# Kernel tuning notes

Hardware: AMD Instinct MI355X
Metric: run time of the kernel (lower is better)

The kernel has to match this reference:

```python
import jax, jax.numpy as jnp
import numpy as np

EPS = 1e-8


def setup_inputs() -> dict:
    key = jax.random.key(0)
    k1, k2, k3 = jax.random.split(key, 3)
    B, K, L, D = 4, 64, 128, 768
    context = jax.random.normal(k1, (B, K, 2, L, D), dtype=jnp.float32)
    # MlpModule(input_size=D): Linear(D, D) -> ReLU -> Linear(D, 1)
    w1 = jax.random.normal(k2, (D, D), dtype=jnp.float32) * (1.0 / np.sqrt(D))
    b1 = jnp.zeros((D,), dtype=jnp.float32)
    w2 = jax.random.normal(k3, (D, 1), dtype=jnp.float32) * (1.0 / np.sqrt(D))
    b2 = jnp.zeros((1,), dtype=jnp.float32)
    return {"context": context, "w1": w1, "b1": b1, "w2": w2, "b2": b2}


def reference(context, w1, b1, w2, b2):
    # context: [B, K, 2, L, D]; slice 0 = context tokens, slice 1 = entity tokens
    ctx = context[:, :, 0, :, :]   # [B, K, L, D]
    ent = context[:, :, 1, :, :]   # [B, K, L, D]

    ctx_norm = jnp.linalg.norm(ctx, axis=-1, keepdims=True)  # [B, K, L, 1]
    ent_norm = jnp.linalg.norm(ent, axis=-1, keepdims=True)  # [B, K, L, 1]

    # cosine-similarity score matrix: [B, K, L, L]
    denom = ctx_norm * jnp.swapaxes(ent_norm, -1, -2) + EPS
    scores = jnp.einsum('bkld,bkmd->bklm', ctx, ent) / denom

    # normalized embeddings (torch code does in-place /= before the stack)
    ctx_n = ctx / ctx_norm
    ent_n = ent / ent_norm

    # top-1 match along entity axis, gather matched entity token per context token
    argmax_idx = jnp.argmax(scores, axis=-1)                       # [B, K, L] int
    matched = jnp.take_along_axis(ent_n, argmax_idx[..., None], axis=2)  # [B, K, L, D]

    pair = jnp.stack([ctx_n, matched], axis=-2)  # [B, K, L, 2, D]

    # MLP: Linear(D,D) -> ReLU -> Linear(D,1), then sum over the pair axis
    h = jax.nn.relu(jnp.einsum('bklpd,de->bklpe', pair, w1) + b1)
    out = jnp.einsum('bklpd,do->bklpo', h, w2) + b2   # [B, K, L, 2, 1]
    out = jnp.sum(out, axis=-2)                        # [B, K, L, 1]
    return jnp.squeeze(out, axis=-1)                   # [B, K, L]
```

## Files before the change

### kernel.cpp

```cpp
#include <hip/hip_runtime.h>
#include <hip/hip_bf16.h>
#include <stdint.h>

#define NB 4
#define NK 64
#define NL 128
#define ND 768
#define NBK (NB*NK)
#define NROW (NBK*NL)
#define LD2 (NL*ND)
#define EPSF 1e-8f
#define THETA 2e-3f
#define CAP 16384

typedef __bf16 bf16x8 __attribute__((ext_vector_type(8)));
typedef float  f32x4  __attribute__((ext_vector_type(4)));

__device__ __forceinline__ int row_off(int r) {
  if (r < NROW) return r*ND + (r >> 7)*LD2;
  int r2 = r - NROW;
  return r2*ND + (r2 >> 7)*LD2 + LD2;
}

__global__ __launch_bounds__(256) void k0_w1t(const float* __restrict__ w1,
                                              __bf16* __restrict__ w1t,
                                              unsigned long long* __restrict__ amax2,
                                              unsigned* __restrict__ cntg) {
  __shared__ float tile[64][68];
  int idx = blockIdx.x*256 + threadIdx.x;
  if (idx < NROW) amax2[idx] = 0ull;
  if (idx == 0) *cntg = 0u;
  int kb = (blockIdx.x / 12) * 64, eb = (blockIdx.x % 12) * 64;
  int t = threadIdx.x;
  int r = t >> 2, c0 = (t & 3) * 16;
  #pragma unroll
  for (int j = 0; j < 4; j++) {
    f32x4 v = *(const f32x4*)(w1 + (kb + r)*ND + eb + c0 + j*4);
    *(f32x4*)&tile[r][c0 + j*4] = v;
  }
  __syncthreads();
  int e = t & 63, gi = t >> 6;
  int eg = eb + e;
  #pragma unroll
  for (int g2 = 0; g2 < 2; g2++) {
    int g = gi*2 + g2;
    bf16x8 o;
    #pragma unroll
    for (int j = 0; j < 8; j++) o[j] = (__bf16)tile[g*8 + j][e];
    int G = (kb >> 3) + (g ^ (eg & 7));
    *(bf16x8*)(w1t + eg*ND + G*8) = o;
  }
}

__device__ __forceinline__ void cvt4(f32x4 v, unsigned& hp0, unsigned& hp1,
                                     unsigned& lp0, unsigned& lp1, float& sq) {
  unsigned u0 = __float_as_uint(v[0]), u1 = __float_as_uint(v[1]);
  unsigned u2 = __float_as_uint(v[2]), u3 = __float_as_uint(v[3]);
  hp0 = (u1 & 0xffff0000u) | (u0 >> 16);
  hp1 = (u3 & 0xffff0000u) | (u2 >> 16);
  float l0 = v[0] - __uint_as_float(u0 & 0xffff0000u);
  float l1 = v[1] - __uint_as_float(u1 & 0xffff0000u);
  float l2 = v[2] - __uint_as_float(u2 & 0xffff0000u);
  float l3 = v[3] - __uint_as_float(u3 & 0xffff0000u);
  lp0 = (__float_as_uint(l1) & 0xffff0000u) | (__float_as_uint(l0) >> 16);
  lp1 = (__float_as_uint(l3) & 0xffff0000u) | (__float_as_uint(l2) >> 16);
  sq += v[0]*v[0] + v[1]*v[1] + v[2]*v[2] + v[3]*v[3];
}

__global__ __launch_bounds__(512) void k2a_screen(
    const float* __restrict__ ctxall, float* __restrict__ norm,
    int* __restrict__ amax, unsigned* __restrict__ cntg,
    unsigned* __restrict__ list) {
  __shared__ alignas(16) __bf16 tiles[2][4][128*32];
  __shared__ float einv_s[128];
  int bk = blockIdx.x;
  int t = threadIdx.x;
  int mat = t >> 8, row = (t >> 1) & 127, kh = (t & 1) * 16;
  const float* src = ctxall + bk*2*LD2 + mat*LD2 + row*ND + kh;
  int w = t >> 6, lane = t & 63, quad = lane >> 4, eloc = lane & 15;

  f32x4 pv[4];
  #pragma unroll
  for (int i = 0; i < 4; i++) pv[i] = *(const f32x4*)(src + i*4);
  float sq = 0.f;
  f32x4 acc[8];
  #pragma unroll
  for (int ct = 0; ct < 8; ct++) acc[ct] = (f32x4){0,0,0,0};

  int p = 0;
  for (int kt = 0; kt < 24; kt++) {
    unsigned h0,h1,h2,h3, l0,l1,l2,l3;
    cvt4(pv[0], h0, h1, l0, l1, sq);
    cvt4(pv[1], h2, h3, l2, l3, sq);
    __bf16* hdst = &tiles[p][2*mat  ][row*32 + kh];
    __bf16* ldst = &tiles[p][2*mat+1][row*32 + kh];
    *(uint4*)hdst = make_uint4(h0,h1,h2,h3);
    *(uint4*)ldst = make_uint4(l0,l1,l2,l3);
    cvt4(pv[2], h0, h1, l0, l1, sq);
    cvt4(pv[3], h2, h3, l2, l3, sq);
    *((uint4*)hdst + 1) = make_uint4(h0,h1,h2,h3);
    *((uint4*)ldst + 1) = make_uint4(l0,l1,l2,l3);
    __syncthreads();
    if (kt < 23) {
      const float* s2 = src + (kt+1)*32;
      #pragma unroll
      for (int i = 0; i < 4; i++) pv[i] = *(const f32x4*)(s2 + i*4);
    }
    bf16x8 ah = *(const bf16x8*)&tiles[p][0][(w*16+eloc)*32 + quad*8];
    bf16x8 al = *(const bf16x8*)&tiles[p][1][(w*16+eloc)*32 + quad*8];
    #pragma unroll
    for (int ct = 0; ct < 8; ct++) {
      bf16x8 bh = *(const bf16x8*)&tiles[p][2][(ct*16+eloc)*32 + quad*8];
      bf16x8 bl = *(const bf16x8*)&tiles[p][3][(ct*16+eloc)*32 + quad*8];
      acc[ct] = __builtin_amdgcn_mfma_f32_16x16x32_bf16(al, bh, acc[ct], 0, 0, 0);
      acc[ct] = __builtin_amdgcn_mfma_f32_16x16x32_bf16(ah, bl, acc[ct], 0, 0, 0);
      acc[ct] = __builtin_amdgcn_mfma_f32_16x16x32_bf16(ah, bh, acc[ct], 0, 0, 0);
    }
    p ^= 1;
  }

  float stot = sq + __shfl_xor(sq, 1);
  if ((t & 1) == 0) {
    float n = sqrtf(stot);
    if (mat == 0) norm[bk*NL + row] = n;
    else { norm[NROW + bk*NL + row] = n; einv_s[row] = 1.0f / n; }
  }
  __syncthreads();

  #pragma unroll
  for (int rr = 0; rr < 4; rr++) {
    float sc[8];
    float best = -3.0e38f; int bcol = 0;
    #pragma unroll
    for (int ct = 0; ct < 8; ct++) {
      sc[ct] = acc[ct][rr] * einv_s[ct*16 + eloc];
      int col = ct*16 + eloc;
      if (sc[ct] > best) { best = sc[ct]; bcol = col; }
    }
    #pragma unroll
    for (int m = 1; m < 16; m <<= 1) {
      float ov = __shfl_xor(best, m);
      int   oc = __shfl_xor(bcol, m);
      if (ov > best || (ov == best && oc < bcol)) { best = ov; bcol = oc; }
    }
    int grow = bk*NL + w*16 + quad*4 + rr;
    if (eloc == 0) amax[grow] = bcol;
    int cnt = 0;
    #pragma unroll
    for (int ct = 0; ct < 8; ct++) cnt += (sc[ct] >= best - THETA) ? 1 : 0;
    #pragma unroll
    for (int m = 1; m < 16; m <<= 1) cnt += __shfl_xor(cnt, m);
    if (cnt >= 2) {
      #pragma unroll
      for (int ct = 0; ct < 8; ct++) {
        if (sc[ct] >= best - THETA) {
          unsigned idx = atomicAdd(cntg, 1u);
          if (idx < CAP) list[idx] = ((unsigned)grow << 7) | (unsigned)(ct*16 + eloc);
        }
      }
    }
  }
}

__global__ __launch_bounds__(256) void k2b_rescore(
    const float* __restrict__ ctxall, const float* __restrict__ norm,
    const unsigned* __restrict__ cntg, const unsigned* __restrict__ list,
    unsigned long long* __restrict__ amax2) {
  unsigned n = *cntg; if (n > CAP) n = CAP;
  int lane = threadIdx.x & 63;
  unsigned wv = blockIdx.x*4 + (threadIdx.x >> 6);
  for (unsigned e = wv; e < n; e += 256) {
    unsigned ent = list[e];
    int row = (int)(ent >> 7), col = (int)(ent & 127);
    int bk = row >> 7;
    const float* a = ctxall + row_off(row);
    const float* b = ctxall + bk*2*LD2 + LD2 + col*ND;
    float d = 0.f;
    #pragma unroll
    for (int i = 0; i < 3; i++) {
      f32x4 va = *(const f32x4*)(a + lane*12 + i*4);
      f32x4 vb = *(const f32x4*)(b + lane*12 + i*4);
      d += va[0]*vb[0] + va[1]*vb[1] + va[2]*vb[2] + va[3]*vb[3];
    }
    #pragma unroll
    for (int m = 1; m < 64; m <<= 1) d += __shfl_xor(d, m);
    if (lane == 0) {
      float cn = norm[row], en = norm[NROW + bk*NL + col];
      float s = d / (cn*en + EPSF);
      unsigned su = __float_as_uint(s);
      unsigned ord = (su & 0x80000000u) ? ~su : (su | 0x80000000u);
      unsigned long long key = ((unsigned long long)ord << 32) | (unsigned)(127 - col);
      atomicMax(&amax2[row], key);
    }
  }
}

__global__ __launch_bounds__(256, 2) void k3_mlp(
    const float* __restrict__ ctxall, const float* __restrict__ norm,
    const __bf16* __restrict__ w1t, const float* __restrict__ b1,
    const float* __restrict__ w2, float* __restrict__ val) {
  __shared__ alignas(16) __bf16 btile[2][16*768];
  int tid = threadIdx.x;
  int wave = tid >> 6, lane = tid & 63;
  int quad = lane >> 4, eloc = lane & 15;
  int rbase = blockIdx.x*128 + wave*32;

  #pragma unroll
  for (int i = 0; i < 6; i++) {
    __builtin_amdgcn_global_load_lds(
      (const __attribute__((address_space(1))) unsigned int*)(w1t + (i*256 + tid)*8),
      (__attribute__((address_space(3))) unsigned int*)(&btile[0][0] + (i*256 + tid)*8),
      16, 0, 0);
  }

  bf16x8 afrag[2][24];
  #pragma unroll
  for (int s = 0; s < 2; s++) {
    int r = rbase + s*16 + eloc;
    const float* src = ctxall + row_off(r);
    float rinv = 1.0f / norm[r];
    #pragma unroll
    for (int ks = 0; ks < 24; ks++) {
      const float* sp = src + ks*32 + quad*8;
      f32x4 v0 = *(const f32x4*)sp;
      f32x4 v1 = *(const f32x4*)(sp + 4);
      bf16x8 a;
      a[0] = (__bf16)(v0[0]*rinv); a[1] = (__bf16)(v0[1]*rinv);
      a[2] = (__bf16)(v0[2]*rinv); a[3] = (__bf16)(v0[3]*rinv);
      a[4] = (__bf16)(v1[0]*rinv); a[5] = (__bf16)(v1[1]*rinv);
      a[6] = (__bf16)(v1[2]*rinv); a[7] = (__bf16)(v1[3]*rinv);
      afrag[s][ks] = a;
    }
  }

  float oacc[2][4] = {{0,0,0,0},{0,0,0,0}};
  int p = 0;
  for (int nt = 0; nt < 48; nt++) {
    __syncthreads();
    if (nt < 47) {
      const __bf16* gsrc = w1t + (nt+1)*16*ND;
      #pragma unroll
      for (int i = 0; i < 6; i++) {
        __builtin_amdgcn_global_load_lds(
          (const __attribute__((address_space(1))) unsigned int*)(gsrc + (i*256 + tid)*8),
          (__attribute__((address_space(3))) unsigned int*)(&btile[p^1][0] + (i*256 + tid)*8),
          16, 0, 0);
      }
    }
    f32x4 h0 = {0,0,0,0}, h1 = {0,0,0,0};
    #pragma unroll
    for (int ks = 0; ks < 24; ks++) {
      int g = ks*4 + quad;
      bf16x8 bfrag = *(const bf16x8*)(&btile[p][0] + eloc*ND + ((g ^ (eloc & 7))*8));
      h0 = __builtin_amdgcn_mfma_f32_16x16x32_bf16(afrag[0][ks], bfrag, h0, 0, 0, 0);
      h1 = __builtin_amdgcn_mfma_f32_16x16x32_bf16(afrag[1][ks], bfrag, h1, 0, 0, 0);
    }
    float b1v = b1[nt*16 + eloc];
    float w2v = w2[nt*16 + eloc];
    #pragma unroll
    for (int rr = 0; rr < 4; rr++) {
      oacc[0][rr] += fmaxf(h0[rr] + b1v, 0.f) * w2v;
      oacc[1][rr] += fmaxf(h1[rr] + b1v, 0.f) * w2v;
    }
    p ^= 1;
  }
  #pragma unroll
  for (int m = 1; m < 16; m <<= 1)
    #pragma unroll
    for (int s = 0; s < 2; s++)
      #pragma unroll
      for (int rr = 0; rr < 4; rr++)
        oacc[s][rr] += __shfl_xor(oacc[s][rr], m);
  if (eloc == 0) {
    #pragma unroll
    for (int s = 0; s < 2; s++)
      #pragma unroll
      for (int rr = 0; rr < 4; rr++)
        val[rbase + s*16 + quad*4 + rr] = oacc[s][rr];
  }
}

__global__ void k4_out(const float* __restrict__ val, const int* __restrict__ amax,
                       const unsigned long long* __restrict__ amax2,
                       const float* __restrict__ b2, float* __restrict__ out) {
  int i = blockIdx.x*256 + threadIdx.x;
  int bk = i >> 7;
  unsigned long long k = amax2[i];
  int a = k ? (127 - (int)(k & 127ull)) : amax[i];
  out[i] = val[i] + val[NROW + bk*NL + a] + 2.0f*b2[0];
}

extern "C" void kernel_launch(void* const* d_in, const int* in_sizes, int n_in,
                              void* d_out, int out_size, void* d_ws, size_t ws_size,
                              hipStream_t stream) {
  const float* ctxall = (const float*)d_in[0];
  const float* w1 = (const float*)d_in[1];
  const float* b1 = (const float*)d_in[2];
  const float* w2 = (const float*)d_in[3];
  const float* b2 = (const float*)d_in[4];
  float* out = (float*)d_out;

  char* ws = (char*)d_ws;
  float*    norm = (float*)ws;
  int*      amax = (int*)(ws + 262144);
  float*    val  = (float*)(ws + 393216);
  __bf16*   w1t  = (__bf16*)(ws + 655360);
  unsigned long long* amax2 = (unsigned long long*)(ws + 1835008);
  unsigned* cntg = (unsigned*)(ws + 2097152);
  unsigned* list = (unsigned*)(ws + 2097156);

  hipLaunchKernelGGL(k0_w1t,     dim3(144),        dim3(256), 0, stream, w1, w1t, amax2, cntg);
  hipLaunchKernelGGL(k2a_screen, dim3(NBK),        dim3(512), 0, stream, ctxall, norm, amax, cntg, list);
  hipLaunchKernelGGL(k2b_rescore,dim3(64),         dim3(256), 0, stream, ctxall, norm, cntg, list, amax2);
  hipLaunchKernelGGL(k3_mlp,     dim3(2*NROW/128), dim3(256), 0, stream, ctxall, norm, w1t, b1, w2, val);
  hipLaunchKernelGGL(k4_out,     dim3(NROW/256),   dim3(256), 0, stream, val, amax, amax2, b2, out);
}
```

Before: 397.7 us.

## Emit bf16 copy of activations in screen kernel and feed MLP from it

New measurement: 431.7 us. 1.09x slower.

```diff
diff --git a/kernel.cpp b/kernel.cpp
--- a/kernel.cpp
+++ b/kernel.cpp
@@ -67,10 +67,17 @@
   sq += v[0]*v[0] + v[1]*v[1] + v[2]*v[2] + v[3]*v[3];
 }
 
+__device__ __forceinline__ bf16x8 rnd8(f32x4 a, f32x4 b) {
+  bf16x8 o;
+  o[0] = (__bf16)a[0]; o[1] = (__bf16)a[1]; o[2] = (__bf16)a[2]; o[3] = (__bf16)a[3];
+  o[4] = (__bf16)b[0]; o[5] = (__bf16)b[1]; o[6] = (__bf16)b[2]; o[7] = (__bf16)b[3];
+  return o;
+}
+
 __global__ __launch_bounds__(512) void k2a_screen(
     const float* __restrict__ ctxall, float* __restrict__ norm,
     int* __restrict__ amax, unsigned* __restrict__ cntg,
-    unsigned* __restrict__ list) {
+    unsigned* __restrict__ list, __bf16* __restrict__ abf16) {
   __shared__ alignas(16) __bf16 tiles[2][4][128*32];
   __shared__ float einv_s[128];
   int bk = blockIdx.x;
@@ -78,6 +85,8 @@
   int mat = t >> 8, row = (t >> 1) & 127, kh = (t & 1) * 16;
   const float* src = ctxall + bk*2*LD2 + mat*LD2 + row*ND + kh;
   int w = t >> 6, lane = t & 63, quad = lane >> 4, eloc = lane & 15;
+  __bf16* arow = abf16 ? (abf16 + (size_t)((mat ? NROW : 0) + bk*NL + row)*ND + kh)
+                       : (__bf16*)0;
 
   f32x4 pv[4];
   #pragma unroll
@@ -96,11 +105,18 @@
     __bf16* ldst = &tiles[p][2*mat+1][row*32 + kh];
     *(uint4*)hdst = make_uint4(h0,h1,h2,h3);
     *(uint4*)ldst = make_uint4(l0,l1,l2,l3);
+    bf16x8 rb0, rb1;
+    if (arow) rb0 = rnd8(pv[0], pv[1]);
     cvt4(pv[2], h0, h1, l0, l1, sq);
     cvt4(pv[3], h2, h3, l2, l3, sq);
     *((uint4*)hdst + 1) = make_uint4(h0,h1,h2,h3);
     *((uint4*)ldst + 1) = make_uint4(l0,l1,l2,l3);
+    if (arow) rb1 = rnd8(pv[2], pv[3]);
     __syncthreads();
+    if (arow) {
+      *(bf16x8*)(arow + kt*32) = rb0;
+      *(bf16x8*)(arow + kt*32 + 8) = rb1;
+    }
     if (kt < 23) {
       const float* s2 = src + (kt+1)*32;
       #pragma unroll
@@ -195,6 +211,84 @@
   }
 }
 
+__global__ __launch_bounds__(512, 2) void k3_mlp_b(
+    const __bf16* __restrict__ abf16, const float* __restrict__ norm,
+    const __bf16* __restrict__ w1t, const float* __restrict__ b1,
+    const float* __restrict__ w2, float* __restrict__ val) {
+  __shared__ alignas(16) __bf16 btile[2][16*768];
+  int tid = threadIdx.x;
+  int wave = tid >> 6, lane = tid & 63;
+  int quad = lane >> 4, eloc = lane & 15;
+  int rbase = blockIdx.x*256 + wave*32;
+
+  #pragma unroll
+  for (int i = 0; i < 3; i++) {
+    __builtin_amdgcn_global_load_lds(
+      (const __attribute__((address_space(1))) unsigned int*)(w1t + (i*512 + tid)*8),
+      (__attribute__((address_space(3))) unsigned int*)(&btile[0][0] + (i*512 + tid)*8),
+      16, 0, 0);
+  }
+
+  bf16x8 afrag[2][24];
+  float rinvv[2][4];
+  #pragma unroll
+  for (int s = 0; s < 2; s++) {
+    const __bf16* src = abf16 + (size_t)(rbase + s*16 + eloc)*ND + quad*8;
+    #pragma unroll
+    for (int ks = 0; ks < 24; ks++)
+      afrag[s][ks] = *(const bf16x8*)(src + ks*32);
+    #pragma unroll
+    for (int rr = 0; rr < 4; rr++)
+      rinvv[s][rr] = 1.0f / norm[rbase + s*16 + quad*4 + rr];
+  }
+
+  float oacc[2][4] = {{0,0,0,0},{0,0,0,0}};
+  int p = 0;
+  for (int nt = 0; nt < 48; nt++) {
+    __syncthreads();
+    if (nt < 47) {
+      const __bf16* gsrc = w1t + (nt+1)*16*ND;
+      #pragma unroll
+      for (int i = 0; i < 3; i++) {
+        __builtin_amdgcn_global_load_lds(
+          (const __attribute__((address_space(1))) unsigned int*)(gsrc + (i*512 + tid)*8),
+          (__attribute__((address_space(3))) unsigned int*)(&btile[p^1][0] + (i*512 + tid)*8),
+          16, 0, 0);
+      }
+    }
+    f32x4 h0 = {0,0,0,0}, h1 = {0,0,0,0};
+    #pragma unroll
+    for (int ks = 0; ks < 24; ks++) {
+      int g = ks*4 + quad;
+      bf16x8 bfrag = *(const bf16x8*)(&btile[p][0] + eloc*ND + ((g ^ (eloc & 7))*8));
+      h0 = __builtin_amdgcn_mfma_f32_16x16x32_bf16(afrag[0][ks], bfrag, h0, 0, 0, 0);
+      h1 = __builtin_amdgcn_mfma_f32_16x16x32_bf16(afrag[1][ks], bfrag, h1, 0, 0, 0);
+    }
+    float b1v = b1[nt*16 + eloc];
+    float w2v = w2[nt*16 + eloc];
+    #pragma unroll
+    for (int rr = 0; rr < 4; rr++) {
+      oacc[0][rr] += fmaxf(h0[rr]*rinvv[0][rr] + b1v, 0.f) * w2v;
+      oacc[1][rr] += fmaxf(h1[rr]*rinvv[1][rr] + b1v, 0.f) * w2v;
+    }
+    p ^= 1;
+  }
+  #pragma unroll
+  for (int m = 1; m < 16; m <<= 1)
+    #pragma unroll
+    for (int s = 0; s < 2; s++)
+      #pragma unroll
+      for (int rr = 0; rr < 4; rr++)
+        oacc[s][rr] += __shfl_xor(oacc[s][rr], m);
+  if (eloc == 0) {
+    #pragma unroll
+    for (int s = 0; s < 2; s++)
+      #pragma unroll
+      for (int rr = 0; rr < 4; rr++)
+        val[rbase + s*16 + quad*4 + rr] = oacc[s][rr];
+  }
+}
+
 __global__ __launch_bounds__(256, 2) void k3_mlp(
     const float* __restrict__ ctxall, const float* __restrict__ norm,
     const __bf16* __restrict__ w1t, const float* __restrict__ b1,
@@ -309,9 +403,18 @@
   unsigned* cntg = (unsigned*)(ws + 2097152);
   unsigned* list = (unsigned*)(ws + 2097156);
 
+  const size_t abf_off = 8ull << 20;
+  const size_t abf_bytes = (size_t)2*NROW*ND*sizeof(__bf16);
+  __bf16* abf16 = (ws_size >= abf_off + abf_bytes) ? (__bf16*)(ws + abf_off)
+                                                   : (__bf16*)0;
+
   hipLaunchKernelGGL(k0_w1t,     dim3(144),        dim3(256), 0, stream, w1, w1t, amax2, cntg);
-  hipLaunchKernelGGL(k2a_screen, dim3(NBK),        dim3(512), 0, stream, ctxall, norm, amax, cntg, list);
+  hipLaunchKernelGGL(k2a_screen, dim3(NBK),        dim3(512), 0, stream, ctxall, norm, amax, cntg, list, abf16);
   hipLaunchKernelGGL(k2b_rescore,dim3(64),         dim3(256), 0, stream, ctxall, norm, cntg, list, amax2);
-  hipLaunchKernelGGL(k3_mlp,     dim3(2*NROW/128), dim3(256), 0, stream, ctxall, norm, w1t, b1, w2, val);
+  if (abf16) {
+    hipLaunchKernelGGL(k3_mlp_b, dim3(2*NROW/256), dim3(512), 0, stream, abf16, norm, w1t, b1, w2, val);
+  } else {
+    hipLaunchKernelGGL(k3_mlp,   dim3(2*NROW/128), dim3(256), 0, stream, ctxall, norm, w1t, b1, w2, val);
+  }
   hipLaunchKernelGGL(k4_out,     dim3(NROW/256),   dim3(256), 0, stream, val, amax, amax2, b2, out);
 }
```

## Split screening kernel into half-row blocks and pad entity tile stride

Applied to the files above, without the earlier changes.

Measured after the change: 393.6 us, median of 2. About the same (-1.0%).

```diff
diff --git a/kernel.cpp b/kernel.cpp
--- a/kernel.cpp
+++ b/kernel.cpp
@@ -12,6 +12,7 @@
 #define EPSF 1e-8f
 #define THETA 2e-3f
 #define CAP 16384
+#define BTS 56
 
 typedef __bf16 bf16x8 __attribute__((ext_vector_type(8)));
 typedef float  f32x4  __attribute__((ext_vector_type(4)));
@@ -67,22 +68,29 @@
   sq += v[0]*v[0] + v[1]*v[1] + v[2]*v[2] + v[3]*v[3];
 }
 
-__global__ __launch_bounds__(512) void k2a_screen(
+__global__ __launch_bounds__(256) void k2a_screen(
     const float* __restrict__ ctxall, float* __restrict__ norm,
     int* __restrict__ amax, unsigned* __restrict__ cntg,
     unsigned* __restrict__ list) {
-  __shared__ alignas(16) __bf16 tiles[2][4][128*32];
+  __shared__ alignas(16) __bf16 Ah[2][64*32], Al[2][64*32];
+  __shared__ alignas(16) __bf16 Bh[2][128*BTS], Bl[2][128*BTS];
   __shared__ float einv_s[128];
-  int bk = blockIdx.x;
+  int bk = blockIdx.x & 255, half = blockIdx.x >> 8;
   int t = threadIdx.x;
-  int mat = t >> 8, row = (t >> 1) & 127, kh = (t & 1) * 16;
-  const float* src = ctxall + bk*2*LD2 + mat*LD2 + row*ND + kh;
   int w = t >> 6, lane = t & 63, quad = lane >> 4, eloc = lane & 15;
-
-  f32x4 pv[4];
-  #pragma unroll
-  for (int i = 0; i < 4; i++) pv[i] = *(const f32x4*)(src + i*4);
-  float sq = 0.f;
+  bool hasA = (t < 128);
+  int srow = t >> 1, kh = (t & 1) * 16;
+  const float* asrc = ctxall + bk*2*LD2 + (half*64 + srow)*ND + kh;
+  const float* bsrc = ctxall + bk*2*LD2 + LD2 + srow*ND + kh;
+
+  f32x4 pa[4], pb[4];
+  #pragma unroll
+  for (int i = 0; i < 4; i++) pb[i] = *(const f32x4*)(bsrc + i*4);
+  if (hasA) {
+    #pragma unroll
+    for (int i = 0; i < 4; i++) pa[i] = *(const f32x4*)(asrc + i*4);
+  }
+  float sqa = 0.f, sqb = 0.f;
   f32x4 acc[8];
   #pragma unroll
   for (int ct = 0; ct < 8; ct++) acc[ct] = (f32x4){0,0,0,0};
@@ -90,28 +98,41 @@
   int p = 0;
   for (int kt = 0; kt < 24; kt++) {
     unsigned h0,h1,h2,h3, l0,l1,l2,l3;
-    cvt4(pv[0], h0, h1, l0, l1, sq);
-    cvt4(pv[1], h2, h3, l2, l3, sq);
-    __bf16* hdst = &tiles[p][2*mat  ][row*32 + kh];
-    __bf16* ldst = &tiles[p][2*mat+1][row*32 + kh];
-    *(uint4*)hdst = make_uint4(h0,h1,h2,h3);
-    *(uint4*)ldst = make_uint4(l0,l1,l2,l3);
-    cvt4(pv[2], h0, h1, l0, l1, sq);
-    cvt4(pv[3], h2, h3, l2, l3, sq);
-    *((uint4*)hdst + 1) = make_uint4(h0,h1,h2,h3);
-    *((uint4*)ldst + 1) = make_uint4(l0,l1,l2,l3);
+    cvt4(pb[0], h0, h1, l0, l1, sqb);
+    cvt4(pb[1], h2, h3, l2, l3, sqb);
+    *(uint4*)&Bh[p][srow*BTS + kh] = make_uint4(h0,h1,h2,h3);
+    *(uint4*)&Bl[p][srow*BTS + kh] = make_uint4(l0,l1,l2,l3);
+    cvt4(pb[2], h0, h1, l0, l1, sqb);
+    cvt4(pb[3], h2, h3, l2, l3, sqb);
+    *((uint4*)&Bh[p][srow*BTS + kh] + 1) = make_uint4(h0,h1,h2,h3);
+    *((uint4*)&Bl[p][srow*BTS + kh] + 1) = make_uint4(l0,l1,l2,l3);
+    if (hasA) {
+      cvt4(pa[0], h0, h1, l0, l1, sqa);
+      cvt4(pa[1], h2, h3, l2, l3, sqa);
+      *(uint4*)&Ah[p][srow*32 + kh] = make_uint4(h0,h1,h2,h3);
+      *(uint4*)&Al[p][srow*32 + kh] = make_uint4(l0,l1,l2,l3);
+      cvt4(pa[2], h0, h1, l0, l1, sqa);
+      cvt4(pa[3], h2, h3, l2, l3, sqa);
+      *((uint4*)&Ah[p][srow*32 + kh] + 1) = make_uint4(h0,h1,h2,h3);
+      *((uint4*)&Al[p][srow*32 + kh] + 1) = make_uint4(l0,l1,l2,l3);
+    }
     __syncthreads();
     if (kt < 23) {
-      const float* s2 = src + (kt+1)*32;
-      #pragma unroll
-      for (int i = 0; i < 4; i++) pv[i] = *(const f32x4*)(s2 + i*4);
-    }
-    bf16x8 ah = *(const bf16x8*)&tiles[p][0][(w*16+eloc)*32 + quad*8];
-    bf16x8 al = *(const bf16x8*)&tiles[p][1][(w*16+eloc)*32 + quad*8];
+      const float* b2 = bsrc + (kt+1)*32;
+      #pragma unroll
+      for (int i = 0; i < 4; i++) pb[i] = *(const f32x4*)(b2 + i*4);
+      if (hasA) {
+        const float* a2 = asrc + (kt+1)*32;
+        #pragma unroll
+        for (int i = 0; i < 4; i++) pa[i] = *(const f32x4*)(a2 + i*4);
+      }
+    }
+    bf16x8 ah = *(const bf16x8*)&Ah[p][(w*16+eloc)*32 + quad*8];
+    bf16x8 al = *(const bf16x8*)&Al[p][(w*16+eloc)*32 + quad*8];
     #pragma unroll
     for (int ct = 0; ct < 8; ct++) {
-      bf16x8 bh = *(const bf16x8*)&tiles[p][2][(ct*16+eloc)*32 + quad*8];
-      bf16x8 bl = *(const bf16x8*)&tiles[p][3][(ct*16+eloc)*32 + quad*8];
+      bf16x8 bh = *(const bf16x8*)&Bh[p][(ct*16+eloc)*BTS + quad*8];
+      bf16x8 bl = *(const bf16x8*)&Bl[p][(ct*16+eloc)*BTS + quad*8];
       acc[ct] = __builtin_amdgcn_mfma_f32_16x16x32_bf16(al, bh, acc[ct], 0, 0, 0);
       acc[ct] = __builtin_amdgcn_mfma_f32_16x16x32_bf16(ah, bl, acc[ct], 0, 0, 0);
       acc[ct] = __builtin_amdgcn_mfma_f32_16x16x32_bf16(ah, bh, acc[ct], 0, 0, 0);
@@ -119,11 +140,15 @@
     p ^= 1;
   }
 
-  float stot = sq + __shfl_xor(sq, 1);
+  float stb = sqb + __shfl_xor(sqb, 1);
   if ((t & 1) == 0) {
-    float n = sqrtf(stot);
-    if (mat == 0) norm[bk*NL + row] = n;
-    else { norm[NROW + bk*NL + row] = n; einv_s[row] = 1.0f / n; }
+    float n = sqrtf(stb);
+    norm[NROW + bk*NL + srow] = n;
+    einv_s[srow] = 1.0f / n;
+  }
+  if (hasA) {
+    float sta = sqa + __shfl_xor(sqa, 1);
+    if ((t & 1) == 0) norm[bk*NL + half*64 + srow] = sqrtf(sta);
   }
   __syncthreads();
 
@@ -143,7 +168,7 @@
       int   oc = __shfl_xor(bcol, m);
       if (ov > best || (ov == best && oc < bcol)) { best = ov; bcol = oc; }
     }
-    int grow = bk*NL + w*16 + quad*4 + rr;
+    int grow = bk*NL + half*64 + w*16 + quad*4 + rr;
     if (eloc == 0) amax[grow] = bcol;
     int cnt = 0;
     #pragma unroll
@@ -310,7 +335,7 @@
   unsigned* list = (unsigned*)(ws + 2097156);
 
   hipLaunchKernelGGL(k0_w1t,     dim3(144),        dim3(256), 0, stream, w1, w1t, amax2, cntg);
-  hipLaunchKernelGGL(k2a_screen, dim3(NBK),        dim3(512), 0, stream, ctxall, norm, amax, cntg, list);
+  hipLaunchKernelGGL(k2a_screen, dim3(2*NBK),      dim3(256), 0, stream, ctxall, norm, amax, cntg, list);
   hipLaunchKernelGGL(k2b_rescore,dim3(64),         dim3(256), 0, stream, ctxall, norm, cntg, list, amax2);
   hipLaunchKernelGGL(k3_mlp,     dim3(2*NROW/128), dim3(256), 0, stream, ctxall, norm, w1t, b1, w2, val);
   hipLaunchKernelGGL(k4_out,     dim3(NROW/256),   dim3(256), 0, stream, val, amax, amax2, b2, out);
```
